# Optimization experiments

Hardware: AMD Instinct MI355X
Metric: run time of the kernel (lower is better)

The kernel has to match this reference:

```python
import jax, jax.numpy as jnp
import numpy as np
from math import pi as PI

L = 8192      # sequence length
D = 512       # feature dim
EMAS = 8      # number of decay rates


def setup_inputs() -> dict:
    key = jax.random.key(0)
    k1, _ = jax.random.split(key)
    x = jax.random.normal(k1, (L, D), dtype=jnp.float32)
    # module initializes log_decay = linspace(-pi, pi, emas)
    log_decay = jnp.linspace(-PI, PI, EMAS, dtype=jnp.float32)
    return {"x": x, "log_decay": log_decay}


def reference(x, log_decay):
    decay = jax.nn.sigmoid(log_decay)               # (emas,)
    # initial state: first element broadcast over emas -> (D, emas)
    state = jnp.broadcast_to(x[0][..., None], x.shape[1:] + (EMAS,))

    def ema_step(ema_0, x_1):
        ema_1 = decay * x_1 + (1.0 - decay) * ema_0
        return ema_1, ema_1

    # scan over l; carries (D, emas), xs is x[..., None] -> (L, D, 1) broadcast against decay
    _, ema_x = jax.lax.scan(ema_step, state, x[..., None])
    return ema_x  # (L, D, emas)
```

## Files before the change

### kernel.cpp

```cpp
#include <hip/hip_runtime.h>
#include <math.h>

#define L_   8192
#define D_   512
#define E_   8
#define DE_  4096
#define C_   256
#define LC_  32
#define TD_  128
#define NF4_ (LC_ * TD_ / 4)
#define P2B_ 64

typedef float f4_t __attribute__((ext_vector_type(4)));

__device__ __forceinline__ float sigmoidf_(float v) {
    return 1.0f / (1.0f + expf(-v));
}

__global__ __launch_bounds__(256) void ema_pass1(const float* __restrict__ x,
                                                 const float* __restrict__ ld,
                                                 float* __restrict__ contrib) {
    __shared__ f4_t tile[NF4_];
    const int c = blockIdx.x >> 2;
    const int q = blockIdx.x & 3;
    const int t = threadIdx.x;

    const f4_t* xg = (const f4_t*)(x + (size_t)c * LC_ * D_ + q * TD_);
#pragma unroll
    for (int k = 0; k < 4; ++k) {
        const int i = t + 256 * k;
        tile[i] = xg[(size_t)(i >> 5) * (D_ / 4) + (i & 31)];
    }

    const int g  = (q << 8) + t;
    const int dl = t >> 1;
    const int eb = (g & 1) << 2;
    float a[4], b[4];
#pragma unroll
    for (int e = 0; e < 4; ++e) { a[e] = sigmoidf_(ld[eb + e]); b[e] = 1.0f - a[e]; }

    __syncthreads();

    const float* tl = (const float*)tile;
    float s[4] = {0.f, 0.f, 0.f, 0.f};
#pragma unroll
    for (int r = 0; r < LC_; ++r) {
        const float xv = tl[r * TD_ + dl];
#pragma unroll
        for (int e = 0; e < 4; ++e) s[e] = fmaf(b[e], s[e], a[e] * xv);
    }
    f4_t rr = {s[0], s[1], s[2], s[3]};
    *(f4_t*)(contrib + (size_t)c * DE_ + 4 * g) = rr;
}

__global__ __launch_bounds__(P2B_) void ema_pass2(const float* __restrict__ x,
                                                  const float* __restrict__ ld,
                                                  const float* __restrict__ contrib,
                                                  float* __restrict__ states) {
    const int chain = blockIdx.x * P2B_ + threadIdx.x;
    const int d = chain >> 3;
    const int e = chain & 7;
    const float a = sigmoidf_(ld[e]);
    float B = 1.0f - a;
#pragma unroll
    for (int k = 0; k < 5; ++k) B *= B;

    float cb[2][32];
#pragma unroll
    for (int j = 0; j < 32; ++j) cb[0][j] = contrib[(size_t)j * DE_ + chain];

    float s = x[d];
    states[chain] = s;

#pragma unroll
    for (int gr = 0; gr < C_ / 32; ++gr) {
        if (gr + 1 < C_ / 32) {
#pragma unroll
            for (int j = 0; j < 32; ++j)
                cb[(gr + 1) & 1][j] = contrib[(size_t)((gr + 1) * 32 + j) * DE_ + chain];
        }
#pragma unroll
        for (int j = 0; j < 32; ++j) {
            s = fmaf(B, s, cb[gr & 1][j]);
            states[(size_t)(gr * 32 + j + 1) * DE_ + chain] = s;
        }
    }
}

__global__ __launch_bounds__(256) void ema_pass3(const float* __restrict__ x,
                                                 const float* __restrict__ ld,
                                                 const float* __restrict__ states,
                                                 float* __restrict__ out) {
    __shared__ f4_t tile[NF4_];
    const int c = blockIdx.x >> 2;
    const int q = blockIdx.x & 3;
    const int t = threadIdx.x;

    const f4_t* xg = (const f4_t*)(x + (size_t)c * LC_ * D_ + q * TD_);
#pragma unroll
    for (int k = 0; k < 4; ++k) {
        const int i = t + 256 * k;
        tile[i] = xg[(size_t)(i >> 5) * (D_ / 4) + (i & 31)];
    }

    const int g  = (q << 8) + t;
    const int dl = t >> 1;
    const int eb = (g & 1) << 2;
    float a[4], b[4];
#pragma unroll
    for (int e = 0; e < 4; ++e) { a[e] = sigmoidf_(ld[eb + e]); b[e] = 1.0f - a[e]; }

    f4_t y = *(const f4_t*)(states + (size_t)c * DE_ + 4 * g);
    float* op = out + (size_t)c * LC_ * DE_ + 4 * g;

    __syncthreads();

    const float* tl = (const float*)tile;
#pragma unroll
    for (int r = 0; r < LC_; ++r) {
        const float xv = tl[r * TD_ + dl];
        y.x = fmaf(b[0], y.x, a[0] * xv);
        y.y = fmaf(b[1], y.y, a[1] * xv);
        y.z = fmaf(b[2], y.z, a[2] * xv);
        y.w = fmaf(b[3], y.w, a[3] * xv);
        __builtin_nontemporal_store(y, (f4_t*)(op + (size_t)r * DE_));
    }
}

__global__ __launch_bounds__(256) void ema_naive(const float* __restrict__ x,
                                                 const float* __restrict__ ld,
                                                 float* __restrict__ out) {
    const int chain = blockIdx.x * 256 + threadIdx.x;
    const int d = chain >> 3;
    const int e = chain & 7;
    const float a = sigmoidf_(ld[e]);
    const float b = 1.0f - a;
    float y = x[d];
    for (int l = 0; l < L_; ++l) {
        y = fmaf(b, y, a * x[(size_t)l * D_ + d]);
        out[(size_t)l * DE_ + chain] = y;
    }
}

extern "C" void kernel_launch(void* const* d_in, const int* in_sizes, int n_in,
                              void* d_out, int out_size, void* d_ws, size_t ws_size,
                              hipStream_t stream) {
    const float* x  = (const float*)d_in[0];
    const float* ld = (const float*)d_in[1];
    float* out = (float*)d_out;

    const size_t need = (size_t)(2 * C_ + 1) * DE_ * sizeof(float);
    if (ws_size >= need) {
        float* contrib = (float*)d_ws;
        float* states  = contrib + (size_t)C_ * DE_;
        ema_pass1<<<C_ * 4, 256, 0, stream>>>(x, ld, contrib);
        ema_pass2<<<DE_ / P2B_, P2B_, 0, stream>>>(x, ld, contrib, states);
        ema_pass3<<<C_ * 4, 256, 0, stream>>>(x, ld, states, out);
    } else {
        ema_naive<<<DE_ / 256, 256, 0, stream>>>(x, ld, out);
    }
}
```

Before: 165.8 us.

## Use full-row chunk blocks with two column halves and lockstep store barriers

Pass 1 and pass 3 now launch one 512-thread block per 32-row chunk instead of four 256-thread blocks per chunk. Each thread handles two feature columns, so every output row is written as one contiguous 16 KB span and x loads are plain contiguous vectors. Pass 3 also adds a barrier after every row's stores to keep the warps in step, which is meant to produce more sequential write traffic. The cost is a quarter as many blocks (256) on a large GPU, 64 KB of shared memory per block, and 32 barriers per block, all of which can cut occupancy and overlap.

```diff
diff --git a/kernel.cpp b/kernel.cpp
--- a/kernel.cpp
+++ b/kernel.cpp
@@ -7,8 +7,7 @@
 #define DE_  4096
 #define C_   256
 #define LC_  32
-#define TD_  128
-#define NF4_ (LC_ * TD_ / 4)
+#define NF4_ (LC_ * D_ / 4)
 #define P2B_ 64
 
 typedef float f4_t __attribute__((ext_vector_type(4)));
@@ -17,24 +16,20 @@
     return 1.0f / (1.0f + expf(-v));
 }
 
-__global__ __launch_bounds__(256) void ema_pass1(const float* __restrict__ x,
+__global__ __launch_bounds__(512) void ema_pass1(const float* __restrict__ x,
                                                  const float* __restrict__ ld,
                                                  float* __restrict__ contrib) {
     __shared__ f4_t tile[NF4_];
-    const int c = blockIdx.x >> 2;
-    const int q = blockIdx.x & 3;
+    const int c = blockIdx.x;
     const int t = threadIdx.x;
 
-    const f4_t* xg = (const f4_t*)(x + (size_t)c * LC_ * D_ + q * TD_);
+    const f4_t* xg = (const f4_t*)(x + (size_t)c * LC_ * D_);
 #pragma unroll
-    for (int k = 0; k < 4; ++k) {
-        const int i = t + 256 * k;
-        tile[i] = xg[(size_t)(i >> 5) * (D_ / 4) + (i & 31)];
-    }
+    for (int k = 0; k < 8; ++k) tile[t + 512 * k] = xg[t + 512 * k];
 
-    const int g  = (q << 8) + t;
-    const int dl = t >> 1;
-    const int eb = (g & 1) << 2;
+    const int dA = t >> 1;
+    const int dB = 256 + (t >> 1);
+    const int eb = (t & 1) << 2;
     float a[4], b[4];
 #pragma unroll
     for (int e = 0; e < 4; ++e) { a[e] = sigmoidf_(ld[eb + e]); b[e] = 1.0f - a[e]; }
@@ -42,15 +37,22 @@
     __syncthreads();
 
     const float* tl = (const float*)tile;
-    float s[4] = {0.f, 0.f, 0.f, 0.f};
+    float sA[4] = {0.f, 0.f, 0.f, 0.f};
+    float sB[4] = {0.f, 0.f, 0.f, 0.f};
 #pragma unroll
     for (int r = 0; r < LC_; ++r) {
-        const float xv = tl[r * TD_ + dl];
+        const float xA = tl[r * D_ + dA];
+        const float xB = tl[r * D_ + dB];
 #pragma unroll
-        for (int e = 0; e < 4; ++e) s[e] = fmaf(b[e], s[e], a[e] * xv);
+        for (int e = 0; e < 4; ++e) {
+            sA[e] = fmaf(b[e], sA[e], a[e] * xA);
+            sB[e] = fmaf(b[e], sB[e], a[e] * xB);
+        }
     }
-    f4_t rr = {s[0], s[1], s[2], s[3]};
-    *(f4_t*)(contrib + (size_t)c * DE_ + 4 * g) = rr;
+    f4_t rA = {sA[0], sA[1], sA[2], sA[3]};
+    f4_t rB = {sB[0], sB[1], sB[2], sB[3]};
+    *(f4_t*)(contrib + (size_t)c * DE_ + 4 * t)        = rA;
+    *(f4_t*)(contrib + (size_t)c * DE_ + 2048 + 4 * t) = rB;
 }
 
 __global__ __launch_bounds__(P2B_) void ema_pass2(const float* __restrict__ x,
@@ -87,43 +89,46 @@
     }
 }
 
-__global__ __launch_bounds__(256) void ema_pass3(const float* __restrict__ x,
+__global__ __launch_bounds__(512) void ema_pass3(const float* __restrict__ x,
                                                  const float* __restrict__ ld,
                                                  const float* __restrict__ states,
                                                  float* __restrict__ out) {
     __shared__ f4_t tile[NF4_];
-    const int c = blockIdx.x >> 2;
-    const int q = blockIdx.x & 3;
+    const int c = blockIdx.x;
     const int t = threadIdx.x;
 
-    const f4_t* xg = (const f4_t*)(x + (size_t)c * LC_ * D_ + q * TD_);
+    const f4_t* xg = (const f4_t*)(x + (size_t)c * LC_ * D_);
 #pragma unroll
-    for (int k = 0; k < 4; ++k) {
-        const int i = t + 256 * k;
-        tile[i] = xg[(size_t)(i >> 5) * (D_ / 4) + (i & 31)];
-    }
+    for (int k = 0; k < 8; ++k) tile[t + 512 * k] = xg[t + 512 * k];
 
-    const int g  = (q << 8) + t;
-    const int dl = t >> 1;
-    const int eb = (g & 1) << 2;
+    const int dA = t >> 1;
+    const int dB = 256 + (t >> 1);
+    const int eb = (t & 1) << 2;
     float a[4], b[4];
 #pragma unroll
     for (int e = 0; e < 4; ++e) { a[e] = sigmoidf_(ld[eb + e]); b[e] = 1.0f - a[e]; }
 
-    f4_t y = *(const f4_t*)(states + (size_t)c * DE_ + 4 * g);
-    float* op = out + (size_t)c * LC_ * DE_ + 4 * g;
+    f4_t yA = *(const f4_t*)(states + (size_t)c * DE_ + 4 * t);
+    f4_t yB = *(const f4_t*)(states + (size_t)c * DE_ + 2048 + 4 * t);
+    float* op = out + (size_t)c * LC_ * DE_ + 4 * t;
 
     __syncthreads();
 
     const float* tl = (const float*)tile;
-#pragma unroll
     for (int r = 0; r < LC_; ++r) {
-        const float xv = tl[r * TD_ + dl];
-        y.x = fmaf(b[0], y.x, a[0] * xv);
-        y.y = fmaf(b[1], y.y, a[1] * xv);
-        y.z = fmaf(b[2], y.z, a[2] * xv);
-        y.w = fmaf(b[3], y.w, a[3] * xv);
-        __builtin_nontemporal_store(y, (f4_t*)(op + (size_t)r * DE_));
+        const float xA = tl[r * D_ + dA];
+        const float xB = tl[r * D_ + dB];
+        yA.x = fmaf(b[0], yA.x, a[0] * xA);
+        yA.y = fmaf(b[1], yA.y, a[1] * xA);
+        yA.z = fmaf(b[2], yA.z, a[2] * xA);
+        yA.w = fmaf(b[3], yA.w, a[3] * xA);
+        yB.x = fmaf(b[0], yB.x, a[0] * xB);
+        yB.y = fmaf(b[1], yB.y, a[1] * xB);
+        yB.z = fmaf(b[2], yB.z, a[2] * xB);
+        yB.w = fmaf(b[3], yB.w, a[3] * xB);
+        __builtin_nontemporal_store(yA, (f4_t*)(op + (size_t)r * DE_));
+        __builtin_nontemporal_store(yB, (f4_t*)(op + (size_t)r * DE_ + 2048));
+        __syncthreads();
     }
 }
 
@@ -153,9 +158,9 @@
     if (ws_size >= need) {
         float* contrib = (float*)d_ws;
         float* states  = contrib + (size_t)C_ * DE_;
-        ema_pass1<<<C_ * 4, 256, 0, stream>>>(x, ld, contrib);
+        ema_pass1<<<C_, 512, 0, stream>>>(x, ld, contrib);
         ema_pass2<<<DE_ / P2B_, P2B_, 0, stream>>>(x, ld, contrib, states);
-        ema_pass3<<<C_ * 4, 256, 0, stream>>>(x, ld, states, out);
+        ema_pass3<<<C_, 512, 0, stream>>>(x, ld, states, out);
     } else {
         ema_naive<<<DE_ / 256, 256, 0, stream>>>(x, ld, out);
     }
```

After: 165.9 us. Within noise of the previous version (+0.1%).
